# Optimization experiments

Measured on AMD Instinct MI355X. Metric: run time of the kernel, lower is better.

## Reference

```python
import jax, jax.numpy as jnp
import numpy as np

D_MODEL = 1024
N_HEADS = 16
D_HEAD = D_MODEL // N_HEADS
B, T = 2, 2048
EPS = 1e-5


def setup_inputs() -> dict:
    key = jax.random.key(0)
    ks = jax.random.split(key, 5)
    s = 1.0 / np.sqrt(D_MODEL)
    return {
        "x": jax.random.normal(ks[0], (B, T, D_MODEL), dtype=jnp.float32),
        "W_q": jax.random.normal(ks[1], (D_MODEL, D_MODEL), dtype=jnp.float32) * s,
        "W_k": jax.random.normal(ks[2], (D_MODEL, D_MODEL), dtype=jnp.float32) * s,
        "W_v": jax.random.normal(ks[3], (D_MODEL, D_MODEL), dtype=jnp.float32) * s,
        "W_o": jax.random.normal(ks[4], (D_MODEL, D_MODEL), dtype=jnp.float32) * s,
        "gn_weight": jnp.ones((D_MODEL,), dtype=jnp.float32),
        "gn_bias": jnp.zeros((D_MODEL,), dtype=jnp.float32),
    }


def reference(x, W_q, W_k, W_v, W_o, gn_weight, gn_bias):
    b, t, dm = x.shape
    h, dh = N_HEADS, D_HEAD
    # per-head decay factors gamma_i = 1 - 2^(-5-i)
    gammas = 1.0 - 2.0 ** (-5.0 - jnp.arange(h, dtype=jnp.float32))  # [H]

    # projections (torch Linear: y = x @ W.T), split heads -> [B,T,H,Dh]
    q = (x @ W_q.T).reshape(b, t, h, dh)
    k = (x @ W_k.T).reshape(b, t, h, dh)
    v = (x @ W_v.T).reshape(b, t, h, dh)

    # causal decay mask D[h,i,j] = gamma_h^(i-j) for i>=j else 0
    idx = jnp.arange(t)
    diff = idx[:, None] - idx[None, :]                      # [T,T]
    pow_ = jnp.maximum(diff, 0).astype(jnp.float32)
    decay = jnp.where(diff >= 0, gammas[:, None, None] ** pow_, 0.0)  # [H,T,T]

    scale = jnp.sqrt(jnp.float32(dh))
    attn = jnp.einsum('bihd,bjhd->bhij', q, k) * decay[None] / scale  # [B,H,T,T]
    y = jnp.einsum('bhij,bjhd->bihd', attn, v)               # [B,T,H,Dh]

    # GroupNorm(n_heads, d_model) over channels-first layout: per (b, head)
    # normalize over (T, d_head)
    mean = y.mean(axis=(1, 3), keepdims=True)
    var = y.var(axis=(1, 3), keepdims=True)
    yn = (y - mean) / jnp.sqrt(var + EPS)
    yn = yn.reshape(b, t, dm) * gn_weight + gn_bias

    return yn @ W_o.T
```

## Files before the change

kernel.cpp:

```cpp
#include <hip/hip_runtime.h>
#include <stdint.h>


#define SEQ 2048

typedef __bf16 bf16x8 __attribute__((ext_vector_type(8)));
typedef float  floatx4 __attribute__((ext_vector_type(4)));
typedef unsigned short ushort4v __attribute__((ext_vector_type(4)));

__device__ __forceinline__ unsigned short f2bf(float f){
    __bf16 h = (__bf16)f;
    return __builtin_bit_cast(unsigned short, h);
}

__device__ __forceinline__ void gload_lds16(const void* g, void* l){
    __builtin_amdgcn_global_load_lds(
        (const __attribute__((address_space(1))) unsigned int*)g,
        (__attribute__((address_space(3))) unsigned int*)l, 16, 0, 0);
}

__global__ __launch_bounds__(256)
void cvt_all(const float* __restrict__ x,
             const float* __restrict__ w0, const float* __restrict__ w1,
             const float* __restrict__ w2, const float* __restrict__ w3,
             unsigned short* __restrict__ xb,
             unsigned short* __restrict__ o0, unsigned short* __restrict__ o1,
             unsigned short* __restrict__ o2, unsigned short* __restrict__ o3,
             float* __restrict__ st){
    const int blk = blockIdx.x;
    if(blk == 0 && threadIdx.x < 128) st[threadIdx.x] = 0.0f;
    const float* src; unsigned short* dst; size_t i;
    if(blk < 4096){ src = x; dst = xb; i = (size_t)blk*256 + threadIdx.x; }
    else {
        const int seg = (blk - 4096) >> 10;
        src = seg==0?w0:seg==1?w1:seg==2?w2:w3;
        dst = seg==0?o0:seg==1?o1:seg==2?o2:o3;
        i = (size_t)((blk - 4096) & 1023)*256 + threadIdx.x;
    }
    float4 v = ((const float4*)src)[i];
    ushort4v o;
    o[0]=f2bf(v.x); o[1]=f2bf(v.y); o[2]=f2bf(v.z); o[3]=f2bf(v.w);
    *(ushort4v*)&dst[i*4] = o;
}

__global__ __launch_bounds__(256, 3)
void gemm_qkv(const unsigned short* __restrict__ A,
              const unsigned short* __restrict__ Wq,
              const unsigned short* __restrict__ Wk,
              const unsigned short* __restrict__ Wv,
              unsigned short* __restrict__ Qo,
              unsigned short* __restrict__ Ko,
              unsigned short* __restrict__ Vo)
{
    __shared__ unsigned short smem[8192];
    unsigned short* As = smem;
    unsigned short* Bs = smem + 4096;
    const int tid  = threadIdx.x;
    const int w    = tid >> 6, lane = tid & 63, q = lane >> 4, cl = lane & 15;
    const int i0   = blockIdx.x * 128;
    const int ysel = blockIdx.y;
    int mode, n0;
    const unsigned short* Bw;
    unsigned short* O;
    if(ysel < 8)      { mode = 0; Bw = Wq; O = Qo; n0 = ysel*128; }
    else if(ysel < 16){ mode = 1; Bw = Wk; O = Ko; n0 = (ysel-8)*128; }
    else              { mode = 2; Bw = Wv; O = Vo; n0 = (ysel-16)*128; }
    const int wm = (w & 1) * 64, wn = (w >> 1) * 64;

    floatx4 acc[4][4];
    #pragma unroll
    for(int a=0;a<4;a++)
        #pragma unroll
        for(int b=0;b<4;b++) acc[a][b] = (floatx4)(0.0f);

    const int srow = lane >> 2;
    const int soff = (lane & 3) * 16;

    for(int k0 = 0; k0 < 1024; k0 += 32){
        __syncthreads();
        #pragma unroll
        for(int t=0;t<2;t++){
            const int ra = (w*2 + t) * 16;
            gload_lds16((const char*)A  + ((size_t)(i0 + ra + srow)*1024 + k0)*2 + soff,
                        (char*)&As[ra*32]);
            gload_lds16((const char*)Bw + ((size_t)(n0 + ra + srow)*1024 + k0)*2 + soff,
                        (char*)&Bs[ra*32]);
        }
        __syncthreads();

        bf16x8 af[4], bfr[4];
        #pragma unroll
        for(int mi=0;mi<4;mi++) af[mi]  = *(const bf16x8*)&As[(wm + mi*16 + cl)*32 + q*8];
        #pragma unroll
        for(int ni=0;ni<4;ni++) bfr[ni] = *(const bf16x8*)&Bs[(wn + ni*16 + cl)*32 + q*8];
        #pragma unroll
        for(int mi=0;mi<4;mi++)
            #pragma unroll
            for(int ni=0;ni<4;ni++)
                acc[mi][ni] = __builtin_amdgcn_mfma_f32_16x16x32_bf16(af[mi], bfr[ni], acc[mi][ni], 0, 0, 0);
    }

    const int b = i0 >> 11;
    if(mode < 2){
        for(int p=0;p<2;p++){
            __syncthreads();
            if((w & 1) == p){
                #pragma unroll
                for(int ni=0;ni<4;ni++){
                    const int h = (n0 + wn + ni*16) >> 6;
                    const float lgh = log2f(1.0f - exp2f(-5.0f - (float)h));
                    const int d = wn + ni*16 + cl, d8 = d >> 3, d7 = d & 7;
                    #pragma unroll
                    for(int mi=0;mi<4;mi++)
                        #pragma unroll
                        for(int r=0;r<4;r++){
                            const int trow = mi*16 + q*4 + r;
                            const int tt = (i0 + p*64 + trow) & 2047;
                            const float sc = (mode==0) ? exp2f((float)tt*lgh)*0.125f
                                                       : exp2f(-(float)tt*lgh);
                            smem[trow*128 + ((d8 ^ (trow & 7))*8) + d7] = f2bf(acc[mi][ni][r]*sc);
                        }
                }
            }
            __syncthreads();
            const int trow = tid >> 2, part = tid & 3;
            const int tt = (i0 + p*64 + trow) & 2047;
            #pragma unroll
            for(int k=0;k<4;k++){
                const int c = k*4 + part;
                bf16x8 vrow = *(const bf16x8*)&smem[trow*128 + ((c ^ (trow & 7))*8)];
                const int h = (n0 + c*8) >> 6, dd = (c*8) & 63;
                *(bf16x8*)&O[(((size_t)(b*16 + h))*2048 + tt)*64 + dd] = vrow;
            }
        }
    } else {
        for(int p=0;p<2;p++){
            __syncthreads();
            if((w >> 1) == p){
                #pragma unroll
                for(int ni=0;ni<4;ni++){
                    const int drow = ni*16 + cl, dr7 = drow & 7;
                    #pragma unroll
                    for(int mi=0;mi<4;mi++){
                        const int t = wm + mi*16 + q*4;
                        const int c = (t >> 3) ^ dr7;
                        ushort4v pk;
                        #pragma unroll
                        for(int r=0;r<4;r++) pk[r] = f2bf(acc[mi][ni][r]);
                        *(ushort4v*)&smem[drow*128 + c*8 + (t & 7)] = pk;
                    }
                }
            }
            __syncthreads();
            const int drow = tid >> 2, part = tid & 3;
            const int dg = n0 + p*64 + drow;
            const int h = dg >> 6, dd = dg & 63;
            const int tbase = i0 & 2047;
            #pragma unroll
            for(int k=0;k<4;k++){
                const int c = k*4 + part;
                bf16x8 vrow = *(const bf16x8*)&smem[drow*128 + ((c ^ (drow & 7))*8)];
                *(bf16x8*)&O[(((size_t)(b*16 + h))*64 + dd)*2048 + tbase + c*8] = vrow;
            }
        }
    }
}

__global__ __launch_bounds__(256, 2)
void retention(const unsigned short* __restrict__ Q,
               const unsigned short* __restrict__ K,
               const unsigned short* __restrict__ VT,
               float* __restrict__ Y0, float* __restrict__ Y1)
{
    __shared__ unsigned short Ks[64*64];
    __shared__ unsigned short Vs[64*64];
    __shared__ unsigned short Ss[4][32*64];

    const int tid = threadIdx.x;
    const int w = tid >> 6, lane = tid & 63, q = lane >> 4, cl = lane & 15;
    const int s = blockIdx.x >> 3, x = blockIdx.x & 7;
    const int bh = blockIdx.y;
    const int wm = w * 32;
    const int l3 = lane >> 3, l7 = lane & 7;
    const int c8 = l7 ^ l3;
    const int cl7 = cl & 7;

    int segbt[2], segjb[2], segje[2], nseg;
    if(s == 0){ nseg = 2;
        segbt[0] = x;     segjb[0] = 0;      segje[0] = 2*x + 2;
        segbt[1] = 15-x;  segjb[1] = 0;      segje[1] = 15 - 2*x;
    } else { nseg = 1;
        segbt[0] = 15-x;  segjb[0] = 15-2*x; segje[0] = 32 - 2*x;
    }

    for(int seg = 0; seg < nseg; seg++){
        const int bt = segbt[seg], jb = segjb[seg], je = segje[seg];
        const int i0 = bt * 128;

        bf16x8 qf[2][2];
        #pragma unroll
        for(int mi=0;mi<2;mi++)
            #pragma unroll
            for(int kk=0;kk<2;kk++)
                qf[mi][kk] = *(const bf16x8*)(Q + ((size_t)bh*SEQ + i0 + wm + mi*16 + cl)*64 + kk*32 + q*8);

        floatx4 Yacc[2][4];
        #pragma unroll
        for(int a=0;a<2;a++)
            #pragma unroll
            for(int b=0;b<4;b++) Yacc[a][b] = (floatx4)(0.0f);

        for(int jt = jb; jt < je; jt++){
            const int j0 = jt * 64;
            __syncthreads();
            #pragma unroll
            for(int t=0;t<2;t++){
                const int r = w*16 + t*8 + l3;
                gload_lds16((const char*)K  + (((size_t)bh*SEQ + j0 + r)*64 + c8*8)*2,
                            (char*)&Ks[(w*16 + t*8)*64]);
                gload_lds16((const char*)VT + (((size_t)bh*64 + r)*SEQ + j0 + c8*8)*2,
                            (char*)&Vs[(w*16 + t*8)*64]);
            }
            __syncthreads();

            floatx4 St[2][4];
            #pragma unroll
            for(int a=0;a<2;a++)
                #pragma unroll
                for(int b=0;b<4;b++) St[a][b] = (floatx4)(0.0f);
            #pragma unroll
            for(int kk=0;kk<2;kk++){
                #pragma unroll
                for(int ni=0;ni<4;ni++){
                    bf16x8 ak = *(const bf16x8*)&Ks[(ni*16 + cl)*64 + ((kk*4+q) ^ cl7)*8];
                    St[0][ni] = __builtin_amdgcn_mfma_f32_16x16x32_bf16(ak, qf[0][kk], St[0][ni], 0,0,0);
                    St[1][ni] = __builtin_amdgcn_mfma_f32_16x16x32_bf16(ak, qf[1][kk], St[1][ni], 0,0,0);
                }
            }

            const bool need_mask = (jt >= 2*bt);
            unsigned short* SsW = Ss[w];
            #pragma unroll
            for(int mi=0;mi<2;mi++){
                const int row = mi*16 + cl;
                const int sw = row & 7;
                const int ig = i0 + wm + row;
                #pragma unroll
                for(int ni=0;ni<4;ni++){
                    ushort4v pk;
                    #pragma unroll
                    for(int r=0;r<4;r++){
                        float v = St[mi][ni][r];
                        if(need_mask){
                            const int jg = j0 + ni*16 + q*4 + r;
                            if(ig < jg) v = 0.0f;
                        }
                        pk[r] = f2bf(v);
                    }
                    *(ushort4v*)&SsW[row*64 + (((ni*2 + (q>>1)) ^ sw)*8) + (q&1)*4] = pk;
                }
            }
            asm volatile("s_waitcnt lgkmcnt(0)" ::: "memory");

            #pragma unroll
            for(int kk=0;kk<2;kk++){
                const int ch = ((kk*4+q) ^ cl7)*8;
                bf16x8 bs0 = *(const bf16x8*)&SsW[( 0 + cl)*64 + ch];
                bf16x8 bs1 = *(const bf16x8*)&SsW[(16 + cl)*64 + ch];
                #pragma unroll
                for(int nt=0;nt<4;nt++){
                    bf16x8 av = *(const bf16x8*)&Vs[(nt*16 + cl)*64 + ch];
                    Yacc[0][nt] = __builtin_amdgcn_mfma_f32_16x16x32_bf16(av, bs0, Yacc[0][nt], 0,0,0);
                    Yacc[1][nt] = __builtin_amdgcn_mfma_f32_16x16x32_bf16(av, bs1, Yacc[1][nt], 0,0,0);
                }
            }
        }

        #pragma unroll
        for(int mi=0;mi<2;mi++)
            #pragma unroll
            for(int nt=0;nt<4;nt++){
                const int ig = i0 + wm + mi*16 + cl;
                #pragma unroll
                for(int r=0;r<4;r++){
                    const int d = nt*16 + q*4 + r;
                    if(s == 0)
                        Y0[((size_t)bh*64 + d)*2048 + ig] = Yacc[mi][nt][r];
                    else
                        Y1[((size_t)bh*64 + d)*1024 + ig - 1024] = Yacc[mi][nt][r];
                }
            }
    }
}

__global__ __launch_bounds__(256)
void gn_stats(const float* __restrict__ Y0, const float* __restrict__ Y1,
              float* __restrict__ st){
    const int g = blockIdx.x >> 3, s8 = blockIdx.x & 7;
    if(g >= 32) return;
    float s1 = 0.f, s2 = 0.f;
    #pragma unroll
    for(int it=0; it<16; it++){
        const int idx = it*256 + threadIdx.x;
        const int dl = idx >> 9;
        const int t4 = idx & 511;
        const int drow = g*64 + s8*8 + dl;
        float4 v = ((const float4*)Y0)[(size_t)drow*512 + t4];
        if(t4 >= 256){
            float4 u = ((const float4*)Y1)[(size_t)drow*256 + t4 - 256];
            v.x += u.x; v.y += u.y; v.z += u.z; v.w += u.w;
        }
        s1 += v.x + v.y + v.z + v.w;
        s2 += v.x*v.x + v.y*v.y + v.z*v.z + v.w*v.w;
    }
    #pragma unroll
    for(int o=32;o>0;o>>=1){ s1 += __shfl_down(s1,o); s2 += __shfl_down(s2,o); }
    __shared__ float r1[4], r2[4];
    const int w = threadIdx.x >> 6, lane = threadIdx.x & 63;
    if(lane == 0){ r1[w] = s1; r2[w] = s2; }
    __syncthreads();
    if(threadIdx.x == 0){
        atomicAdd(&st[g*2+0], r1[0]+r1[1]+r1[2]+r1[3]);
        atomicAdd(&st[g*2+1], r2[0]+r2[1]+r2[2]+r2[3]);
    }
}

__global__ __launch_bounds__(256)
void gn_norm(const float* __restrict__ Y0, const float* __restrict__ Y1,
             const float* __restrict__ st,
             const float* __restrict__ gw, const float* __restrict__ gb,
             unsigned short* __restrict__ Out){
    __shared__ unsigned short T[64*72];
    const int g = blockIdx.x >> 5;
    if(g >= 32) return;
    const int t0 = (blockIdx.x & 31) * 64;
    const int h = g & 15, b = g >> 4;
    const float mean = st[g*2+0] * (1.0f/131072.0f);
    const float var  = st[g*2+1] * (1.0f/131072.0f) - mean*mean;
    const float inv  = rsqrtf(var + 1e-5f);
    const int tid = threadIdx.x;
    const bool hi = (t0 >= 1024);
    #pragma unroll
    for(int kk=0;kk<4;kk++){
        const int f4 = kk*256 + tid;
        const int d = f4 >> 4;
        const int t4l = f4 & 15;
        float4 v = ((const float4*)Y0)[(size_t)(g*64 + d)*512 + (t0>>2) + t4l];
        if(hi){
            float4 u = ((const float4*)Y1)[(size_t)(g*64 + d)*256 + ((t0-1024)>>2) + t4l];
            v.x += u.x; v.y += u.y; v.z += u.z; v.w += u.w;
        }
        const int c = h*64 + d;
        const float sc = inv * gw[c];
        const float bs = gb[c] - mean*sc;
        const int tl = t4l*4;
        T[(tl+0)*72 + d] = f2bf(v.x*sc + bs);
        T[(tl+1)*72 + d] = f2bf(v.y*sc + bs);
        T[(tl+2)*72 + d] = f2bf(v.z*sc + bs);
        T[(tl+3)*72 + d] = f2bf(v.w*sc + bs);
    }
    __syncthreads();
    #pragma unroll
    for(int it=0; it<2; it++){
        const int idx = it*256 + tid;
        const int tl = idx >> 3, segp = idx & 7;
        bf16x8 vrow = *(const bf16x8*)&T[tl*72 + segp*8];
        *(bf16x8*)&Out[((size_t)(b*2048 + t0 + tl))*1024 + h*64 + segp*8] = vrow;
    }
}

__global__ __launch_bounds__(256, 3)
void gemm_out(const unsigned short* __restrict__ A,
              const unsigned short* __restrict__ Bw,
              float* __restrict__ O)
{
    __shared__ unsigned short As[128*32];
    __shared__ unsigned short Bs[64*32];
    const int tid = threadIdx.x;
    const int w = tid >> 6, lane = tid & 63, q = lane >> 4, cl = lane & 15;
    const int i0 = blockIdx.x * 128, n0 = blockIdx.y * 64;
    const int wm = (w & 1) * 64, wn = (w >> 1) * 32;

    floatx4 acc[4][2];
    #pragma unroll
    for(int a=0;a<4;a++)
        #pragma unroll
        for(int b=0;b<2;b++) acc[a][b] = (floatx4)(0.0f);

    const int srow = lane >> 2;
    const int soff = (lane & 3) * 16;

    for(int k0 = 0; k0 < 1024; k0 += 32){
        __syncthreads();
        #pragma unroll
        for(int t=0;t<2;t++){
            const int ra = w*32 + t*16;
            gload_lds16((const char*)A + ((size_t)(i0 + ra + srow)*1024 + k0)*2 + soff,
                        (char*)&As[ra*32]);
        }
        gload_lds16((const char*)Bw + ((size_t)(n0 + w*16 + srow)*1024 + k0)*2 + soff,
                    (char*)&Bs[(w*16)*32]);
        __syncthreads();

        bf16x8 af[4], bfr[2];
        #pragma unroll
        for(int mi=0;mi<4;mi++) af[mi]  = *(const bf16x8*)&As[(wm + mi*16 + cl)*32 + q*8];
        #pragma unroll
        for(int ni=0;ni<2;ni++) bfr[ni] = *(const bf16x8*)&Bs[(wn + ni*16 + cl)*32 + q*8];
        #pragma unroll
        for(int mi=0;mi<4;mi++)
            #pragma unroll
            for(int ni=0;ni<2;ni++)
                acc[mi][ni] = __builtin_amdgcn_mfma_f32_16x16x32_bf16(af[mi], bfr[ni], acc[mi][ni], 0, 0, 0);
    }

    #pragma unroll
    for(int mi=0;mi<4;mi++)
        #pragma unroll
        for(int ni=0;ni<2;ni++){
            const int gi = i0 + wm + mi*16 + q*4;
            const int gn = n0 + wn + ni*16 + cl;
            #pragma unroll
            for(int r=0;r<4;r++) O[(size_t)(gi + r)*1024 + gn] = acc[mi][ni][r];
        }
}

extern "C" void kernel_launch(void* const* d_in, const int* in_sizes, int n_in,
                              void* d_out, int out_size, void* d_ws, size_t ws_size,
                              hipStream_t stream){
    const float* x  = (const float*)d_in[0];
    const float* Wq = (const float*)d_in[1];
    const float* Wk = (const float*)d_in[2];
    const float* Wv = (const float*)d_in[3];
    const float* Wo = (const float*)d_in[4];
    const float* gw = (const float*)d_in[5];
    const float* gb = (const float*)d_in[6];

    char* ws = (char*)d_ws;
    unsigned short* xb  = (unsigned short*)(ws + ((size_t) 0<<20));
    unsigned short* wqb = (unsigned short*)(ws + ((size_t) 8<<20));
    unsigned short* wkb = (unsigned short*)(ws + ((size_t)10<<20));
    unsigned short* wvb = (unsigned short*)(ws + ((size_t)12<<20));
    unsigned short* wob = (unsigned short*)(ws + ((size_t)14<<20));
    unsigned short* qb  = (unsigned short*)(ws + ((size_t)16<<20));
    unsigned short* kb  = (unsigned short*)(ws + ((size_t)24<<20));
    unsigned short* vtb = (unsigned short*)(ws + ((size_t)32<<20));
    float*          y0  = (float*)         (ws + ((size_t)40<<20));
    unsigned short* ynb = (unsigned short*)(ws + ((size_t)56<<20));
    float*          y1  = (float*)         (ws + ((size_t) 0<<20));
    float*          st  = (float*)         (ws + ((size_t)64<<20));

    cvt_all<<<8192, 256, 0, stream>>>(x, Wq, Wk, Wv, Wo, xb, wqb, wkb, wvb, wob, st);

    gemm_qkv<<<dim3(32,24,1), 256, 0, stream>>>(xb, wqb, wkb, wvb, qb, kb, vtb);

    retention<<<dim3(16,32,1), 256, 0, stream>>>(qb, kb, vtb, y0, y1);

    gn_stats<<<256, 256, 0, stream>>>(y0, y1, st);
    gn_norm<<<1024, 256, 0, stream>>>(y0, y1, st, gw, gb, ynb);

    gemm_out<<<dim3(32,16,1), 256, 0, stream>>>(ynb, wob, (float*)d_out);
}
```

Baseline: 188.7 us.

## Widen retention key tiles to 128 and single-pass QKV GEMM epilogue

The retention kernel now processes 128 keys per iteration instead of 64, which halves the loop trips and barriers per query block. To support this, the K/V/S shared buffers are enlarged and a new swizzle handles the wider rows. The QKV GEMM epilogue writes the whole 128x128 tile to a doubled shared buffer in one pass instead of two. It also computes the decay scales by repeated multiplication of gamma powers instead of one exp2 per element. The cost is more LDS per block in both kernels, which may reduce occupancy, and the masked diagonal tile now does more wasted work.

```diff
diff --git a/kernel.cpp b/kernel.cpp
--- a/kernel.cpp
+++ b/kernel.cpp
@@ -52,7 +52,7 @@
               unsigned short* __restrict__ Ko,
               unsigned short* __restrict__ Vo)
 {
-    __shared__ unsigned short smem[8192];
+    __shared__ unsigned short smem[16384];
     unsigned short* As = smem;
     unsigned short* Bs = smem + 4096;
     const int tid  = threadIdx.x;
@@ -101,66 +101,79 @@
     }
 
     const int b = i0 >> 11;
+    const int tb = i0 & 2047;
+    __syncthreads();
+
     if(mode < 2){
-        for(int p=0;p<2;p++){
-            __syncthreads();
-            if((w & 1) == p){
-                #pragma unroll
-                for(int ni=0;ni<4;ni++){
-                    const int h = (n0 + wn + ni*16) >> 6;
-                    const float lgh = log2f(1.0f - exp2f(-5.0f - (float)h));
-                    const int d = wn + ni*16 + cl, d8 = d >> 3, d7 = d & 7;
-                    #pragma unroll
-                    for(int mi=0;mi<4;mi++)
-                        #pragma unroll
-                        for(int r=0;r<4;r++){
-                            const int trow = mi*16 + q*4 + r;
-                            const int tt = (i0 + p*64 + trow) & 2047;
-                            const float sc = (mode==0) ? exp2f((float)tt*lgh)*0.125f
-                                                       : exp2f(-(float)tt*lgh);
-                            smem[trow*128 + ((d8 ^ (trow & 7))*8) + d7] = f2bf(acc[mi][ni][r]*sc);
-                        }
-                }
-            }
-            __syncthreads();
-            const int trow = tid >> 2, part = tid & 3;
-            const int tt = (i0 + p*64 + trow) & 2047;
+        const int h = (n0 + wn) >> 6;
+        const float gamma = 1.0f - __builtin_ldexpf(1.0f, -5 - h);
+        const float lgh = log2f(gamma);
+        float g1p, base;
+        if(mode == 0){ g1p = gamma;        base = exp2f((float)tb * lgh) * 0.125f; }
+        else         { g1p = 1.0f / gamma; base = exp2f(-(float)tb * lgh); }
+        const float g2 = g1p*g1p, g4 = g2*g2, g8 = g4*g4, g16 = g8*g8;
+        const float g32 = g16*g16, g64 = g32*g32;
+        float sq = base;
+        if(q & 1) sq *= g4;
+        if(q & 2) sq *= g8;
+        if(wm)    sq *= g64;
+
+        #pragma unroll
+        for(int ni=0;ni<4;ni++){
+            const int d = wn + ni*16 + cl, d8 = d >> 3, d7 = d & 7;
+            float cur = sq;
+            #pragma unroll
+            for(int mi=0;mi<4;mi++){
+                const int tr0 = wm + mi*16 + q*4;
+                float v0 = cur, v1 = v0*g1p, v2 = v1*g1p, v3 = v2*g1p;
+                smem[(tr0+0)*128 + ((d8 ^ ((tr0+0)&7))*8) + d7] = f2bf(acc[mi][ni][0]*v0);
+                smem[(tr0+1)*128 + ((d8 ^ ((tr0+1)&7))*8) + d7] = f2bf(acc[mi][ni][1]*v1);
+                smem[(tr0+2)*128 + ((d8 ^ ((tr0+2)&7))*8) + d7] = f2bf(acc[mi][ni][2]*v2);
+                smem[(tr0+3)*128 + ((d8 ^ ((tr0+3)&7))*8) + d7] = f2bf(acc[mi][ni][3]*v3);
+                cur *= g16;
+            }
+        }
+        __syncthreads();
+        const int part = tid & 3;
+        #pragma unroll
+        for(int rr=0;rr<2;rr++){
+            const int row = (tid>>2)*2 + rr;
+            const int tt = tb + row;
             #pragma unroll
             for(int k=0;k<4;k++){
                 const int c = k*4 + part;
-                bf16x8 vrow = *(const bf16x8*)&smem[trow*128 + ((c ^ (trow & 7))*8)];
-                const int h = (n0 + c*8) >> 6, dd = (c*8) & 63;
-                *(bf16x8*)&O[(((size_t)(b*16 + h))*2048 + tt)*64 + dd] = vrow;
+                bf16x8 vrow = *(const bf16x8*)&smem[row*128 + ((c ^ (row&7))*8)];
+                const int h2 = (n0 + c*8) >> 6, dd = (c*8) & 63;
+                *(bf16x8*)&O[(((size_t)(b*16 + h2))*2048 + tt)*64 + dd] = vrow;
             }
         }
     } else {
-        for(int p=0;p<2;p++){
-            __syncthreads();
-            if((w >> 1) == p){
-                #pragma unroll
-                for(int ni=0;ni<4;ni++){
-                    const int drow = ni*16 + cl, dr7 = drow & 7;
-                    #pragma unroll
-                    for(int mi=0;mi<4;mi++){
-                        const int t = wm + mi*16 + q*4;
-                        const int c = (t >> 3) ^ dr7;
-                        ushort4v pk;
-                        #pragma unroll
-                        for(int r=0;r<4;r++) pk[r] = f2bf(acc[mi][ni][r]);
-                        *(ushort4v*)&smem[drow*128 + c*8 + (t & 7)] = pk;
-                    }
-                }
-            }
-            __syncthreads();
-            const int drow = tid >> 2, part = tid & 3;
-            const int dg = n0 + p*64 + drow;
-            const int h = dg >> 6, dd = dg & 63;
-            const int tbase = i0 & 2047;
+        #pragma unroll
+        for(int ni=0;ni<4;ni++){
+            const int drow = wn + ni*16 + cl, dr7 = drow & 7;
+            #pragma unroll
+            for(int mi=0;mi<4;mi++){
+                const int ch = (wm>>3) + mi*2 + (q>>1);
+                const int phys = (ch & 8) | ((ch & 7) ^ dr7);
+                ushort4v pk;
+                #pragma unroll
+                for(int r=0;r<4;r++) pk[r] = f2bf(acc[mi][ni][r]);
+                *(ushort4v*)&smem[drow*128 + phys*8 + (q&1)*4] = pk;
+            }
+        }
+        __syncthreads();
+        const int part = tid & 3;
+        #pragma unroll
+        for(int rr=0;rr<2;rr++){
+            const int row = (tid>>2)*2 + rr;
+            const int dg = n0 + row;
+            const int h2 = dg >> 6, dd = dg & 63;
             #pragma unroll
             for(int k=0;k<4;k++){
                 const int c = k*4 + part;
-                bf16x8 vrow = *(const bf16x8*)&smem[drow*128 + ((c ^ (drow & 7))*8)];
-                *(bf16x8*)&O[(((size_t)(b*16 + h))*64 + dd)*2048 + tbase + c*8] = vrow;
+                const int phys = (c & 8) | ((c & 7) ^ (row & 7));
+                bf16x8 vrow = *(const bf16x8*)&smem[row*128 + phys*8];
+                *(bf16x8*)&O[(((size_t)(b*16 + h2))*64 + dd)*2048 + tb + c*8] = vrow;
             }
         }
     }
@@ -172,9 +185,9 @@
                const unsigned short* __restrict__ VT,
                float* __restrict__ Y0, float* __restrict__ Y1)
 {
-    __shared__ unsigned short Ks[64*64];
-    __shared__ unsigned short Vs[64*64];
-    __shared__ unsigned short Ss[4][32*64];
+    __shared__ unsigned short Ks[128*64];
+    __shared__ unsigned short Vs[64*128];
+    __shared__ unsigned short Ss[4][32*128];
 
     const int tid = threadIdx.x;
     const int w = tid >> 6, lane = tid & 63, q = lane >> 4, cl = lane & 15;
@@ -182,15 +195,14 @@
     const int bh = blockIdx.y;
     const int wm = w * 32;
     const int l3 = lane >> 3, l7 = lane & 7;
-    const int c8 = l7 ^ l3;
     const int cl7 = cl & 7;
 
     int segbt[2], segjb[2], segje[2], nseg;
     if(s == 0){ nseg = 2;
-        segbt[0] = x;     segjb[0] = 0;      segje[0] = 2*x + 2;
-        segbt[1] = 15-x;  segjb[1] = 0;      segje[1] = 15 - 2*x;
+        segbt[0] = x;     segjb[0] = 0;     segje[0] = x + 1;
+        segbt[1] = 15-x;  segjb[1] = 0;     segje[1] = 8 - x;
     } else { nseg = 1;
-        segbt[0] = 15-x;  segjb[0] = 15-2*x; segje[0] = 32 - 2*x;
+        segbt[0] = 15-x;  segjb[0] = 8-x;   segje[0] = 16 - x;
     }
 
     for(int seg = 0; seg < nseg; seg++){
@@ -211,34 +223,40 @@
             for(int b=0;b<4;b++) Yacc[a][b] = (floatx4)(0.0f);
 
         for(int jt = jb; jt < je; jt++){
-            const int j0 = jt * 64;
+            const int j0 = jt * 128;
             __syncthreads();
             #pragma unroll
-            for(int t=0;t<2;t++){
-                const int r = w*16 + t*8 + l3;
-                gload_lds16((const char*)K  + (((size_t)bh*SEQ + j0 + r)*64 + c8*8)*2,
-                            (char*)&Ks[(w*16 + t*8)*64]);
-                gload_lds16((const char*)VT + (((size_t)bh*64 + r)*SEQ + j0 + c8*8)*2,
-                            (char*)&Vs[(w*16 + t*8)*64]);
+            for(int t=0;t<4;t++){
+                const int r = w*32 + t*8 + l3;
+                gload_lds16((const char*)K + (((size_t)bh*SEQ + j0 + r)*64 + (l7^l3)*8)*2,
+                            (char*)&Ks[(w*32 + t*8)*64]);
+            }
+            #pragma unroll
+            for(int t=0;t<4;t++){
+                const int r = w*16 + t*4 + (lane>>4);
+                const int pc = lane & 15;
+                const int cc = (pc & 8) | ((pc & 7) ^ (r & 7));
+                gload_lds16((const char*)VT + (((size_t)bh*64 + r)*SEQ + j0 + cc*8)*2,
+                            (char*)&Vs[(w*16 + t*4)*128]);
             }
             __syncthreads();
 
-            floatx4 St[2][4];
+            floatx4 St[2][8];
             #pragma unroll
             for(int a=0;a<2;a++)
                 #pragma unroll
-                for(int b=0;b<4;b++) St[a][b] = (floatx4)(0.0f);
+                for(int b=0;b<8;b++) St[a][b] = (floatx4)(0.0f);
             #pragma unroll
             for(int kk=0;kk<2;kk++){
                 #pragma unroll
-                for(int ni=0;ni<4;ni++){
+                for(int ni=0;ni<8;ni++){
                     bf16x8 ak = *(const bf16x8*)&Ks[(ni*16 + cl)*64 + ((kk*4+q) ^ cl7)*8];
                     St[0][ni] = __builtin_amdgcn_mfma_f32_16x16x32_bf16(ak, qf[0][kk], St[0][ni], 0,0,0);
                     St[1][ni] = __builtin_amdgcn_mfma_f32_16x16x32_bf16(ak, qf[1][kk], St[1][ni], 0,0,0);
                 }
             }
 
-            const bool need_mask = (jt >= 2*bt);
+            const bool need_mask = (jt == bt);
             unsigned short* SsW = Ss[w];
             #pragma unroll
             for(int mi=0;mi<2;mi++){
@@ -246,7 +264,9 @@
                 const int sw = row & 7;
                 const int ig = i0 + wm + row;
                 #pragma unroll
-                for(int ni=0;ni<4;ni++){
+                for(int ni=0;ni<8;ni++){
+                    const int jc = ni*2 + (q>>1);
+                    const int phys = (jc & 8) | ((jc & 7) ^ sw);
                     ushort4v pk;
                     #pragma unroll
                     for(int r=0;r<4;r++){
@@ -257,19 +277,20 @@
                         }
                         pk[r] = f2bf(v);
                     }
-                    *(ushort4v*)&SsW[row*64 + (((ni*2 + (q>>1)) ^ sw)*8) + (q&1)*4] = pk;
+                    *(ushort4v*)&SsW[row*128 + phys*8 + (q&1)*4] = pk;
                 }
             }
             asm volatile("s_waitcnt lgkmcnt(0)" ::: "memory");
 
             #pragma unroll
-            for(int kk=0;kk<2;kk++){
-                const int ch = ((kk*4+q) ^ cl7)*8;
-                bf16x8 bs0 = *(const bf16x8*)&SsW[( 0 + cl)*64 + ch];
-                bf16x8 bs1 = *(const bf16x8*)&SsW[(16 + cl)*64 + ch];
+            for(int kk=0;kk<4;kk++){
+                const int c = kk*4 + q;
+                const int phys = (c & 8) | ((c & 7) ^ cl7);
+                bf16x8 bs0 = *(const bf16x8*)&SsW[( 0 + cl)*128 + phys*8];
+                bf16x8 bs1 = *(const bf16x8*)&SsW[(16 + cl)*128 + phys*8];
                 #pragma unroll
                 for(int nt=0;nt<4;nt++){
-                    bf16x8 av = *(const bf16x8*)&Vs[(nt*16 + cl)*64 + ch];
+                    bf16x8 av = *(const bf16x8*)&Vs[(nt*16 + cl)*128 + phys*8];
                     Yacc[0][nt] = __builtin_amdgcn_mfma_f32_16x16x32_bf16(av, bs0, Yacc[0][nt], 0,0,0);
                     Yacc[1][nt] = __builtin_amdgcn_mfma_f32_16x16x32_bf16(av, bs1, Yacc[1][nt], 0,0,0);
                 }
```

Result: no change. 188.8 us (+0.0%).
